# Optimization experiments

Measured on AMD Instinct MI355X. Metric: run time of the kernel, lower is better.

Reference implementation:

```python
import jax, jax.numpy as jnp
import numpy as np

EMBED_DIM = 2048
NUM_HEADS = 32
NUM_KV_HEADS = 8
HEAD_DIM = EMBED_DIM // NUM_HEADS
KV_REPEAT = NUM_HEADS // NUM_KV_HEADS
ROPE_BASE = 10000.0


def rotate_half(x):
    # interleaved rotate: (-x_odd, x_even) re-interleaved on last dim
    x_even = x[..., ::2]
    x_odd = x[..., 1::2]
    return jnp.stack((-x_odd, x_even), axis=-1).reshape(x.shape)


def rope_cos_sin(seq_len, dtype, start_pos=0):
    inv_freq = 1.0 / (ROPE_BASE ** (jnp.arange(0, HEAD_DIM, 2, dtype=jnp.float32) / HEAD_DIM))
    pos = jnp.arange(start_pos, start_pos + seq_len, dtype=jnp.float32)
    freqs = jnp.outer(pos, inv_freq)  # [T, head_dim/2]
    cos = jnp.repeat(jnp.cos(freqs), 2, axis=-1).astype(dtype)  # [T, head_dim]
    sin = jnp.repeat(jnp.sin(freqs), 2, axis=-1).astype(dtype)
    return cos[None, None], sin[None, None]  # [1,1,T,head_dim]


def setup_inputs() -> dict:
    key = jax.random.key(0)
    ks = jax.random.split(key, 5)
    s = 0.02
    x = jax.random.normal(ks[0], (2, 2048, EMBED_DIM), dtype=jnp.float32)
    Wq = jax.random.normal(ks[1], (EMBED_DIM, EMBED_DIM), dtype=jnp.float32) * s
    Wk = jax.random.normal(ks[2], (EMBED_DIM, NUM_KV_HEADS * HEAD_DIM), dtype=jnp.float32) * s
    Wv = jax.random.normal(ks[3], (EMBED_DIM, NUM_KV_HEADS * HEAD_DIM), dtype=jnp.float32) * s
    Wo = jax.random.normal(ks[4], (EMBED_DIM, EMBED_DIM), dtype=jnp.float32) * s
    return {
        "x": x,
        "Wq": Wq, "bq": jnp.zeros((EMBED_DIM,), jnp.float32),
        "Wk": Wk, "bk": jnp.zeros((NUM_KV_HEADS * HEAD_DIM,), jnp.float32),
        "Wv": Wv, "bv": jnp.zeros((NUM_KV_HEADS * HEAD_DIM,), jnp.float32),
        "Wo": Wo, "bo": jnp.zeros((EMBED_DIM,), jnp.float32),
    }


def reference(x, Wq, bq, Wk, bk, Wv, bv, Wo, bo):
    B, T, C = x.shape
    q = (x @ Wq + bq).reshape(B, T, NUM_HEADS, HEAD_DIM).transpose(0, 2, 1, 3)      # [B,H,T,D]
    k = (x @ Wk + bk).reshape(B, T, NUM_KV_HEADS, HEAD_DIM).transpose(0, 2, 1, 3)   # [B,Hkv,T,D]
    v = (x @ Wv + bv).reshape(B, T, NUM_KV_HEADS, HEAD_DIM).transpose(0, 2, 1, 3)

    cos, sin = rope_cos_sin(T, q.dtype, start_pos=0)
    q = q * cos + rotate_half(q) * sin
    k = k * cos + rotate_half(k) * sin

    # GQA: repeat KV heads to match query heads (faithful to repeat_interleave)
    k_rep = jnp.repeat(k, KV_REPEAT, axis=1)  # [B,H,T,D]
    v_rep = jnp.repeat(v, KV_REPEAT, axis=1)

    scale = np.sqrt(HEAD_DIM).astype(np.float32)
    scores = jnp.einsum('bhqd,bhkd->bhqk', q, k_rep) / scale  # [B,H,T,T]

    # causal mask: key_pos > query_pos -> -inf
    qpos = jnp.arange(T)[:, None]
    kpos = jnp.arange(T)[None, :]
    scores = jnp.where((kpos > qpos)[None, None], -jnp.inf, scores)

    attn = jax.nn.softmax(scores, axis=-1)
    out = jnp.einsum('bhqk,bhkd->bhqd', attn, v_rep)  # [B,H,T,D]
    out = out.transpose(0, 2, 1, 3).reshape(B, T, C)
    return out @ Wo + bo
```

## Files before the change

kernel.cpp:

```cpp
#include <hip/hip_runtime.h>
#include <hip/hip_bf16.h>
#include <stdint.h>
#include <stddef.h>

#define EMBED 2048
#define TLEN  2048
#define BSZ   2
#define NH    32
#define NKV   8
#define HD    64
#define MROWS (BSZ*TLEN)
#define KVD   (NKV*HD)
#define QKVN  3072

typedef __attribute__((ext_vector_type(8))) short   s16x8;
typedef __attribute__((ext_vector_type(4))) short   s16x4;
typedef __attribute__((ext_vector_type(8))) __bf16  bf16x8;
typedef __attribute__((ext_vector_type(4))) float   f32x4;
typedef __attribute__((ext_vector_type(2))) unsigned long long u64x2;
typedef __attribute__((ext_vector_type(4))) uint32_t u32x4;

static __device__ __forceinline__ float bf2f(short u) {
  union { float f; uint32_t i; } c; c.i = ((uint32_t)(uint16_t)u) << 16; return c.f;
}
static __device__ __forceinline__ short f2bf(float f) {
  union { float f; uint32_t i; } c; c.f = f;
  uint32_t x = c.i;
  uint32_t r = (x + 0x7fffu + ((x >> 16) & 1u)) >> 16;
  return (short)(uint16_t)r;
}
static __device__ __forceinline__ bf16x8 as_bf16x8(s16x8 s) {
  return __builtin_bit_cast(bf16x8, s);
}
static __device__ __forceinline__ bf16x8 mk8(unsigned long long a, unsigned long long b) {
  u64x2 t; t.x = a; t.y = b;
  return __builtin_bit_cast(bf16x8, t);
}
static __device__ __forceinline__ bf16x8 mk8w(uint32_t w0, uint32_t w1,
                                              uint32_t w2, uint32_t w3) {
  u32x4 t; t.x = w0; t.y = w1; t.z = w2; t.w = w3;
  return __builtin_bit_cast(bf16x8, t);
}

__device__ __forceinline__ void transpose_tile(
    const float* __restrict__ W, short* __restrict__ Wt, int N,
    int bx, int by, int tx, int ty) {
  __shared__ float tile[32][33];
  const int n0 = bx * 32, k0 = by * 32;
  #pragma unroll
  for (int i = 0; i < 32; i += 8)
    tile[ty + i][tx] = W[(size_t)(k0 + ty + i) * N + n0 + tx];
  __syncthreads();
  #pragma unroll
  for (int i = 0; i < 32; i += 8)
    Wt[(size_t)(n0 + ty + i) * 2048 + k0 + tx] = f2bf(tile[tx][ty + i]);
}

__global__ __launch_bounds__(256) void prep_kernel(
    const float* __restrict__ Wq, const float* __restrict__ Wk,
    const float* __restrict__ Wv, const float* __restrict__ Wo,
    const float* __restrict__ x,
    short* __restrict__ WqkvT, short* __restrict__ WoT,
    short* __restrict__ xb, float2* __restrict__ tab) {
  const int bid = blockIdx.x;
  const int tid = threadIdx.x;
  const int tx = tid & 31, ty = tid >> 5;
  if (bid < 4096) {
    transpose_tile(Wq, WqkvT, 2048, bid & 63, bid >> 6, tx, ty);
  } else if (bid < 5120) {
    const int l = bid - 4096;
    transpose_tile(Wk, WqkvT + (size_t)2048 * 2048, 512, l & 15, l >> 4, tx, ty);
  } else if (bid < 6144) {
    const int l = bid - 5120;
    transpose_tile(Wv, WqkvT + (size_t)2560 * 2048, 512, l & 15, l >> 4, tx, ty);
  } else if (bid < 10240) {
    const int l = bid - 6144;
    transpose_tile(Wo, WoT, 2048, l & 63, l >> 6, tx, ty);
  } else if (bid < 18432) {
    const int i = ((bid - 10240) * 256 + tid) * 4;
    f32x4 v = *(const f32x4*)(x + i);
    s16x4 o = { f2bf(v.x), f2bf(v.y), f2bf(v.z), f2bf(v.w) };
    *(s16x4*)(xb + i) = o;
  } else {
    const int idx = (bid - 18432) * 256 + tid;
    const int t = idx >> 5, i = idx & 31;
    float ang = (float)t * powf(10000.0f, -(float)i / 32.0f);
    float c, s;
    sincosf(ang, &c, &s);
    tab[idx] = make_float2(c, s);
  }
}

__global__ __launch_bounds__(256) void rope_fused_kernel(
    short* __restrict__ QKV, const float2* __restrict__ tab) {
  const int idx = blockIdx.x * 256 + threadIdx.x;
  const int row = idx / 320;
  const int c8 = (idx - row * 320) * 8;
  const float QSC = 0.125f * 1.44269504088896340736f;
  const float sc = (c8 < 2048) ? QSC : 1.0f;
  const int t = row & (TLEN - 1);
  const int i0 = (c8 & 63) >> 1;
  const float4* tp = (const float4*)&tab[(t << 5) + i0];
  const float4 cs01 = tp[0], cs23 = tp[1];
  short* p = QKV + (size_t)row * QKVN + c8;
  s16x8 v = *(const s16x8*)p;
  const float e0 = bf2f(v[0]), o0 = bf2f(v[1]), e1 = bf2f(v[2]), o1 = bf2f(v[3]);
  const float e2 = bf2f(v[4]), o2 = bf2f(v[5]), e3 = bf2f(v[6]), o3 = bf2f(v[7]);
  s16x8 r;
  r[0] = f2bf((e0 * cs01.x + o0 * cs01.y) * sc);
  r[1] = f2bf((o0 * cs01.x - e0 * cs01.y) * sc);
  r[2] = f2bf((e1 * cs01.z + o1 * cs01.w) * sc);
  r[3] = f2bf((o1 * cs01.z - e1 * cs01.w) * sc);
  r[4] = f2bf((e2 * cs23.x + o2 * cs23.y) * sc);
  r[5] = f2bf((o2 * cs23.x - e2 * cs23.y) * sc);
  r[6] = f2bf((e3 * cs23.z + o3 * cs23.w) * sc);
  r[7] = f2bf((o3 * cs23.z - e3 * cs23.w) * sc);
  *(s16x8*)p = r;
}

template<bool OUT_F32, bool TRIPLE_BIAS>
__global__ __launch_bounds__(256) void gemm_bt(
    const short* __restrict__ A, const short* __restrict__ Bt,
    const float* __restrict__ b0, const float* __restrict__ b1,
    const float* __restrict__ b2, void* __restrict__ Cout, int ldc) {
  const int K = 2048;
  __shared__ __align__(16) short As[128 * 32];
  __shared__ __align__(16) short Bs[128 * 32];
  int bn = blockIdx.x, bm = blockIdx.y;
  int tid = threadIdx.x;
  int lane = tid & 63, wave = tid >> 6;
  int wr = wave >> 1, wc = wave & 1;
  int fr = lane & 15, fk = lane >> 4;
  f32x4 acc[4][4] = {};
  const short* Ab = A + (size_t)bm * 128 * K;
  const short* Bb = Bt + (size_t)bn * 128 * K;
  for (int kt = 0; kt < K; kt += 32) {
    #pragma unroll
    for (int ii = 0; ii < 2; ++ii) {
      const int i = wave * 2 + ii;
      const int r = i * 16 + (lane >> 2);
      const int c = lane & 3;
      const size_t go = (size_t)r * K + kt + c * 8;
      __builtin_amdgcn_global_load_lds(
          (const __attribute__((address_space(1))) void*)(Ab + go),
          (__attribute__((address_space(3))) void*)&As[i * 512], 16, 0, 0);
      __builtin_amdgcn_global_load_lds(
          (const __attribute__((address_space(1))) void*)(Bb + go),
          (__attribute__((address_space(3))) void*)&Bs[i * 512], 16, 0, 0);
    }
    __syncthreads();
    bf16x8 af[4], bfr[4];
    #pragma unroll
    for (int m = 0; m < 4; ++m)
      af[m] = as_bf16x8(*(const s16x8*)&As[(wr * 64 + m * 16 + fr) * 32 + fk * 8]);
    #pragma unroll
    for (int n = 0; n < 4; ++n)
      bfr[n] = as_bf16x8(*(const s16x8*)&Bs[(wc * 64 + n * 16 + fr) * 32 + fk * 8]);
    __builtin_amdgcn_s_setprio(1);
    #pragma unroll
    for (int m = 0; m < 4; ++m)
      #pragma unroll
      for (int n = 0; n < 4; ++n)
        acc[m][n] = __builtin_amdgcn_mfma_f32_16x16x32_bf16(af[m], bfr[n], acc[m][n], 0, 0, 0);
    __builtin_amdgcn_s_setprio(0);
    __syncthreads();
  }
  int row0 = bm * 128 + wr * 64;
  int col0 = bn * 128 + wc * 64;
  #pragma unroll
  for (int n = 0; n < 4; ++n) {
    int col = col0 + n * 16 + fr;
    float bv;
    if constexpr (TRIPLE_BIAS)
      bv = (col < 2048) ? b0[col] : ((col < 2560) ? b1[col - 2048] : b2[col - 2560]);
    else
      bv = b0[col];
    #pragma unroll
    for (int m = 0; m < 4; ++m)
      #pragma unroll
      for (int j = 0; j < 4; ++j) {
        int row = row0 + m * 16 + fk * 4 + j;
        float v = acc[m][n][j] + bv;
        if constexpr (OUT_F32) ((float*)Cout)[(size_t)row * ldc + col] = v;
        else                   ((short*)Cout)[(size_t)row * ldc + col] = f2bf(v);
      }
  }
}

__global__ __launch_bounds__(256) void attn_kernel(
    const short* __restrict__ Q, const short* __restrict__ Kx,
    const short* __restrict__ Vx, short* __restrict__ O) {
  const int pr = blockIdx.x;
  const int bh = blockIdx.y;
  const int b = bh >> 5, h = bh & 31, kvh = h >> 2;
  const int tid = threadIdx.x;
  const int lane = tid & 63, wave = tid >> 6;
  const int fr = lane & 15, fk = lane >> 4;

  __shared__ __align__(16) short Ks[64][72];
  __shared__ __align__(16) short VS[4 * 1040];

  const short* Kbase = Kx + (size_t)b * TLEN * QKVN + kvh * HD;
  const short* Vbase = Vx + (size_t)b * TLEN * QKVN + kvh * HD;

  const int srow = tid >> 3;
  const int scb  = (tid & 7) << 3;
  const int vd0  = scb >> 4;
  const int vco  = scb & 15;
  const int p0 = (((srow >> 2) & 3) << 3) | (((srow >> 4) & 1) << 2) | (srow & 3);
  const int vaddr0 = vd0 * 1040 + ((p0 >> 2) << 6) + ((p0 & 3) << 4) + vco;
  const int vaddr1 = vaddr0 + 512;
  const unsigned trb = (unsigned)(unsigned long long)&VS[fk * 128 + fr * 4];
  const bf16x8 ones = mk8(0x3F803F803F803F80ULL, 0x3F803F803F803F80ULL);

#define TRREAD(dst, OFF) asm volatile("ds_read_b64_tr_b16 %0, %1 offset:" OFF \
    : "=v"(dst) : "v"(trb) : "memory")
#define CVTPK(d, lo, hi) asm volatile("v_cvt_pk_bf16_f32 %0, %1, %2" \
    : "=v"(d) : "v"(lo), "v"(hi))

  #pragma unroll 1
  for (int rep = 0; rep < 2; ++rep) {
    const int qt = rep ? (31 - pr) : pr;
    const int q0 = qt * 64;
    const short* Qrow = Q + (size_t)(b * TLEN + q0 + wave * 16 + fr) * QKVN + h * HD;
    const bf16x8 aq0 = as_bf16x8(*(const s16x8*)&Qrow[fk * 8]);
    const bf16x8 aq1 = as_bf16x8(*(const s16x8*)&Qrow[32 + fk * 8]);
    f32x4 oacc[4] = {};
    f32x4 lacc = {};
    float m = -INFINITY;
    const int qloc = wave * 16 + fr;

    for (int kv0 = 0; kv0 <= q0; kv0 += 64) {
      #pragma unroll
      for (int it = 0; it < 2; ++it) {
        const int r = srow + it * 32;
        const size_t gro = (size_t)(kv0 + r) * QKVN + scb;
        *(s16x8*)&Ks[r][scb] = *(const s16x8*)&Kbase[gro];
        s16x8 vv = *(const s16x8*)&Vbase[gro];
        *(s16x8*)&VS[it ? vaddr1 : vaddr0] = vv;
      }
      __syncthreads();

      f32x4 sacc[4] = {};
      {
        bf16x8 bk0[4], bk1[4];
        #pragma unroll
        for (int mb = 0; mb < 4; ++mb) {
          bk0[mb] = as_bf16x8(*(const s16x8*)&Ks[mb * 16 + fr][fk * 8]);
          bk1[mb] = as_bf16x8(*(const s16x8*)&Ks[mb * 16 + fr][32 + fk * 8]);
        }
        __builtin_amdgcn_s_setprio(1);
        #pragma unroll
        for (int mb = 0; mb < 4; ++mb) {
          sacc[mb] = __builtin_amdgcn_mfma_f32_16x16x32_bf16(bk0[mb], aq0, sacc[mb], 0, 0, 0);
          sacc[mb] = __builtin_amdgcn_mfma_f32_16x16x32_bf16(bk1[mb], aq1, sacc[mb], 0, 0, 0);
        }
        __builtin_amdgcn_s_setprio(0);
      }

      const bool diag = (kv0 == q0);
      float sv[4][4];
      float pm = -INFINITY;
      #pragma unroll
      for (int mb = 0; mb < 4; ++mb)
        #pragma unroll
        for (int j = 0; j < 4; ++j) {
          float v = sacc[mb][j];
          if (diag && (mb * 16 + fk * 4 + j > qloc)) v = -INFINITY;
          sv[mb][j] = v;
          pm = fmaxf(pm, v);
        }
      pm = fmaxf(pm, __shfl_xor(pm, 16, 64));
      pm = fmaxf(pm, __shfl_xor(pm, 32, 64));

      if (__any(pm > m + 11.5f)) {
        const float mnew = fmaxf(m, pm);
        const float al = exp2f(m - mnew);
        m = mnew;
        lacc[0] *= al; lacc[1] *= al; lacc[2] *= al; lacc[3] *= al;
        #pragma unroll
        for (int db = 0; db < 4; ++db) {
          oacc[db][0] *= al; oacc[db][1] *= al;
          oacc[db][2] *= al; oacc[db][3] *= al;
        }
      }

      uint32_t rlo[4], rhi[4];
      #pragma unroll
      for (int mb = 0; mb < 4; ++mb) {
        float e0 = exp2f(sv[mb][0] - m);
        float e1 = exp2f(sv[mb][1] - m);
        float e2 = exp2f(sv[mb][2] - m);
        float e3 = exp2f(sv[mb][3] - m);
        CVTPK(rlo[mb], e0, e1);
        CVTPK(rhi[mb], e2, e3);
      }
      const bf16x8 pB0 = mk8w(rlo[0], rhi[0], rlo[1], rhi[1]);
      const bf16x8 pB1 = mk8w(rlo[2], rhi[2], rlo[3], rhi[3]);

      unsigned long long t00, t01, t02, t03, t10, t11, t12, t13;
      unsigned long long t20, t21, t22, t23, t30, t31, t32, t33;
      TRREAD(t00, "0");    TRREAD(t01, "128");  TRREAD(t02, "1024"); TRREAD(t03, "1152");
      TRREAD(t10, "2080"); TRREAD(t11, "2208"); TRREAD(t12, "3104"); TRREAD(t13, "3232");
      TRREAD(t20, "4160"); TRREAD(t21, "4288"); TRREAD(t22, "5184"); TRREAD(t23, "5312");
      TRREAD(t30, "6240"); TRREAD(t31, "6368"); TRREAD(t32, "7264"); TRREAD(t33, "7392");
      asm volatile("s_waitcnt lgkmcnt(0)" ::: "memory");
      __builtin_amdgcn_sched_barrier(0);
      __builtin_amdgcn_s_setprio(1);
      lacc = __builtin_amdgcn_mfma_f32_16x16x32_bf16(ones, pB0, lacc, 0, 0, 0);
      lacc = __builtin_amdgcn_mfma_f32_16x16x32_bf16(ones, pB1, lacc, 0, 0, 0);
      oacc[0] = __builtin_amdgcn_mfma_f32_16x16x32_bf16(mk8(t00, t01), pB0, oacc[0], 0, 0, 0);
      oacc[0] = __builtin_amdgcn_mfma_f32_16x16x32_bf16(mk8(t02, t03), pB1, oacc[0], 0, 0, 0);
      oacc[1] = __builtin_amdgcn_mfma_f32_16x16x32_bf16(mk8(t10, t11), pB0, oacc[1], 0, 0, 0);
      oacc[1] = __builtin_amdgcn_mfma_f32_16x16x32_bf16(mk8(t12, t13), pB1, oacc[1], 0, 0, 0);
      oacc[2] = __builtin_amdgcn_mfma_f32_16x16x32_bf16(mk8(t20, t21), pB0, oacc[2], 0, 0, 0);
      oacc[2] = __builtin_amdgcn_mfma_f32_16x16x32_bf16(mk8(t22, t23), pB1, oacc[2], 0, 0, 0);
      oacc[3] = __builtin_amdgcn_mfma_f32_16x16x32_bf16(mk8(t30, t31), pB0, oacc[3], 0, 0, 0);
      oacc[3] = __builtin_amdgcn_mfma_f32_16x16x32_bf16(mk8(t32, t33), pB1, oacc[3], 0, 0, 0);
      __builtin_amdgcn_s_setprio(0);
      __syncthreads();
    }

    {
      const float linv = 1.0f / lacc[0];
      short* orow = O + (size_t)(b * TLEN + q0 + wave * 16 + fr) * EMBED + h * HD + fk * 4;
      #pragma unroll
      for (int db = 0; db < 4; ++db) {
        s16x4 o4 = { f2bf(oacc[db][0] * linv), f2bf(oacc[db][1] * linv),
                     f2bf(oacc[db][2] * linv), f2bf(oacc[db][3] * linv) };
        *(s16x4*)&orow[db * 16] = o4;
      }
    }
  }
#undef TRREAD
#undef CVTPK
}

extern "C" void kernel_launch(void* const* d_in, const int* in_sizes, int n_in,
                              void* d_out, int out_size, void* d_ws, size_t ws_size,
                              hipStream_t stream) {
  const float* x  = (const float*)d_in[0];
  const float* Wq = (const float*)d_in[1];
  const float* bq = (const float*)d_in[2];
  const float* Wk = (const float*)d_in[3];
  const float* bk = (const float*)d_in[4];
  const float* Wv = (const float*)d_in[5];
  const float* bv = (const float*)d_in[6];
  const float* Wo = (const float*)d_in[7];
  const float* bo = (const float*)d_in[8];
  float* out = (float*)d_out;

  char* ws = (char*)d_ws;
  short* xb    = (short*)(ws);
  short* WqkvT = (short*)(ws + 16777216);
  short* WoT   = (short*)(ws + 29360128);
  short* QKV   = (short*)(ws + 37748736);
  short* Ob    = (short*)(ws);
  float2* tab  = (float2*)d_out;

  prep_kernel<<<18688, 256, 0, stream>>>(Wq, Wk, Wv, Wo, x, WqkvT, WoT, xb, tab);

  gemm_bt<false, true><<<dim3(QKVN / 128, MROWS / 128), 256, 0, stream>>>(
      xb, WqkvT, bq, bk, bv, QKV, QKVN);

  rope_fused_kernel<<<(MROWS * 320) / 256, 256, 0, stream>>>(QKV, tab);

  attn_kernel<<<dim3(16, BSZ * NH), 256, 0, stream>>>(
      QKV, QKV + 2048, QKV + 2560, Ob);

  gemm_bt<true, false><<<dim3(EMBED / 128, MROWS / 128), 256, 0, stream>>>(
      Ob, WoT, bo, bo, bo, out, EMBED);
}
```

Before: 228.2 us.

## Double-buffer K/V tiles in attention with register prefetch

Attention now keeps two LDS buffers for K and V tiles. The next tile's global loads are issued into registers before the QK/softmax/PV compute and written to the other buffer afterward, so load latency overlaps with MFMA work and one barrier per iteration goes away. The cost is more LDS per block, which may lower occupancy, and extra registers held across the loop for the prefetched data.

```diff
diff --git a/kernel.cpp b/kernel.cpp
--- a/kernel.cpp
+++ b/kernel.cpp
@@ -197,8 +197,8 @@
   const int lane = tid & 63, wave = tid >> 6;
   const int fr = lane & 15, fk = lane >> 4;
 
-  __shared__ __align__(16) short Ks[64][72];
-  __shared__ __align__(16) short VS[4 * 1040];
+  __shared__ __align__(16) short Ks[2][64][72];
+  __shared__ __align__(16) short VS[2][4160];
 
   const short* Kbase = Kx + (size_t)b * TLEN * QKVN + kvh * HD;
   const short* Vbase = Vx + (size_t)b * TLEN * QKVN + kvh * HD;
@@ -210,13 +210,15 @@
   const int p0 = (((srow >> 2) & 3) << 3) | (((srow >> 4) & 1) << 2) | (srow & 3);
   const int vaddr0 = vd0 * 1040 + ((p0 >> 2) << 6) + ((p0 & 3) << 4) + vco;
   const int vaddr1 = vaddr0 + 512;
-  const unsigned trb = (unsigned)(unsigned long long)&VS[fk * 128 + fr * 4];
+  const unsigned trbase = (unsigned)(unsigned long long)&VS[0][fk * 128 + fr * 4];
   const bf16x8 ones = mk8(0x3F803F803F803F80ULL, 0x3F803F803F803F80ULL);
 
-#define TRREAD(dst, OFF) asm volatile("ds_read_b64_tr_b16 %0, %1 offset:" OFF \
-    : "=v"(dst) : "v"(trb) : "memory")
+#define TRREAD(dst, BASE, OFF) asm volatile("ds_read_b64_tr_b16 %0, %1 offset:" OFF \
+    : "=v"(dst) : "v"(BASE) : "memory")
 #define CVTPK(d, lo, hi) asm volatile("v_cvt_pk_bf16_f32 %0, %1, %2" \
     : "=v"(d) : "v"(lo), "v"(hi))
+
+  int cur = 0;
 
   #pragma unroll 1
   for (int rep = 0; rep < 2; ++rep) {
@@ -230,24 +232,40 @@
     float m = -INFINITY;
     const int qloc = wave * 16 + fr;
 
+    {
+      const size_t g0 = (size_t)srow * QKVN + scb;
+      const size_t g1 = (size_t)(srow + 32) * QKVN + scb;
+      s16x8 ka = *(const s16x8*)&Kbase[g0];
+      s16x8 kb = *(const s16x8*)&Kbase[g1];
+      s16x8 va = *(const s16x8*)&Vbase[g0];
+      s16x8 vb = *(const s16x8*)&Vbase[g1];
+      *(s16x8*)&Ks[cur][srow][scb] = ka;
+      *(s16x8*)&Ks[cur][srow + 32][scb] = kb;
+      *(s16x8*)&VS[cur][vaddr0] = va;
+      *(s16x8*)&VS[cur][vaddr1] = vb;
+    }
+    __syncthreads();
+
     for (int kv0 = 0; kv0 <= q0; kv0 += 64) {
-      #pragma unroll
-      for (int it = 0; it < 2; ++it) {
-        const int r = srow + it * 32;
-        const size_t gro = (size_t)(kv0 + r) * QKVN + scb;
-        *(s16x8*)&Ks[r][scb] = *(const s16x8*)&Kbase[gro];
-        s16x8 vv = *(const s16x8*)&Vbase[gro];
-        *(s16x8*)&VS[it ? vaddr1 : vaddr0] = vv;
-      }
-      __syncthreads();
+      const bool more = (kv0 + 64 <= q0);
+
+      s16x8 ka, kb, va, vb;
+      if (more) {
+        const size_t g0 = (size_t)(kv0 + 64 + srow) * QKVN + scb;
+        const size_t g1 = (size_t)(kv0 + 64 + srow + 32) * QKVN + scb;
+        ka = *(const s16x8*)&Kbase[g0];
+        kb = *(const s16x8*)&Kbase[g1];
+        va = *(const s16x8*)&Vbase[g0];
+        vb = *(const s16x8*)&Vbase[g1];
+      }
 
       f32x4 sacc[4] = {};
       {
         bf16x8 bk0[4], bk1[4];
         #pragma unroll
         for (int mb = 0; mb < 4; ++mb) {
-          bk0[mb] = as_bf16x8(*(const s16x8*)&Ks[mb * 16 + fr][fk * 8]);
-          bk1[mb] = as_bf16x8(*(const s16x8*)&Ks[mb * 16 + fr][32 + fk * 8]);
+          bk0[mb] = as_bf16x8(*(const s16x8*)&Ks[cur][mb * 16 + fr][fk * 8]);
+          bk1[mb] = as_bf16x8(*(const s16x8*)&Ks[cur][mb * 16 + fr][32 + fk * 8]);
         }
         __builtin_amdgcn_s_setprio(1);
         #pragma unroll
@@ -298,12 +316,17 @@
       const bf16x8 pB0 = mk8w(rlo[0], rhi[0], rlo[1], rhi[1]);
       const bf16x8 pB1 = mk8w(rlo[2], rhi[2], rlo[3], rhi[3]);
 
+      const unsigned trb = trbase + (unsigned)(cur * 8320);
       unsigned long long t00, t01, t02, t03, t10, t11, t12, t13;
       unsigned long long t20, t21, t22, t23, t30, t31, t32, t33;
-      TRREAD(t00, "0");    TRREAD(t01, "128");  TRREAD(t02, "1024"); TRREAD(t03, "1152");
-      TRREAD(t10, "2080"); TRREAD(t11, "2208"); TRREAD(t12, "3104"); TRREAD(t13, "3232");
-      TRREAD(t20, "4160"); TRREAD(t21, "4288"); TRREAD(t22, "5184"); TRREAD(t23, "5312");
-      TRREAD(t30, "6240"); TRREAD(t31, "6368"); TRREAD(t32, "7264"); TRREAD(t33, "7392");
+      TRREAD(t00, trb, "0");    TRREAD(t01, trb, "128");
+      TRREAD(t02, trb, "1024"); TRREAD(t03, trb, "1152");
+      TRREAD(t10, trb, "2080"); TRREAD(t11, trb, "2208");
+      TRREAD(t12, trb, "3104"); TRREAD(t13, trb, "3232");
+      TRREAD(t20, trb, "4160"); TRREAD(t21, trb, "4288");
+      TRREAD(t22, trb, "5184"); TRREAD(t23, trb, "5312");
+      TRREAD(t30, trb, "6240"); TRREAD(t31, trb, "6368");
+      TRREAD(t32, trb, "7264"); TRREAD(t33, trb, "7392");
       asm volatile("s_waitcnt lgkmcnt(0)" ::: "memory");
       __builtin_amdgcn_sched_barrier(0);
       __builtin_amdgcn_s_setprio(1);
@@ -318,7 +341,15 @@
       oacc[3] = __builtin_amdgcn_mfma_f32_16x16x32_bf16(mk8(t30, t31), pB0, oacc[3], 0, 0, 0);
       oacc[3] = __builtin_amdgcn_mfma_f32_16x16x32_bf16(mk8(t32, t33), pB1, oacc[3], 0, 0, 0);
       __builtin_amdgcn_s_setprio(0);
+
+      if (more) {
+        *(s16x8*)&Ks[cur ^ 1][srow][scb] = ka;
+        *(s16x8*)&Ks[cur ^ 1][srow + 32][scb] = kb;
+        *(s16x8*)&VS[cur ^ 1][vaddr0] = va;
+        *(s16x8*)&VS[cur ^ 1][vaddr1] = vb;
+      }
       __syncthreads();
+      cur ^= 1;
     }
 
     {
```

Result: slower. 245.0 us (+7.4%).
